# Performance work log

Hardware: AMD Instinct MI355X
Metric: run time of the kernel (lower is better)

Reference implementation:

```python
import jax, jax.numpy as jnp
import numpy as np

B, S, H, T = 32, 1024, 1024, 256
WINDOW = 2
ITERATIONS = 3


def setup_inputs() -> dict:
    key = jax.random.key(0)
    k1, k2, k3, k4, k5, k6 = jax.random.split(key, 6)
    token_feats = jax.random.normal(k1, (B, S, H), dtype=jnp.float32)
    unary_score = jax.random.normal(k2, (B, S, T), dtype=jnp.float32)
    lengths = jax.random.randint(k3, (B,), S // 2, S + 1)  # in [S/2, S]
    mask = (jnp.arange(S)[None, :] < lengths[:, None]).astype(jnp.float32)
    transitions = jax.random.normal(k4, (WINDOW, T, T), dtype=jnp.float32)
    start_transitions = jax.random.normal(k5, (WINDOW, T), dtype=jnp.float32)
    end_transitions = jax.random.normal(k6, (WINDOW, T), dtype=jnp.float32)
    return {
        "token_feats": token_feats,
        "unary_score": unary_score,
        "mask": mask,
        "transitions": transitions,
        "start_transitions": start_transitions,
        "end_transitions": end_transitions,
        "lengths": lengths,
    }


def reference(token_feats, unary_score, mask, transitions, start_transitions,
              end_transitions, lengths):
    # mask unary (and token_feats, as in original; token_feats is unused in
    # the plain-transitions second-order path)
    unary = unary_score * mask[..., None]        # [B,S,T]
    _ = token_feats * mask[..., None]
    q = unary
    batch_range = jnp.arange(q.shape[0])
    for _it in range(ITERATIONS):
        q = jax.nn.softmax(q, axis=-1)
        left_sum = jnp.zeros_like(q)
        right_sum = jnp.zeros_like(q)
        for j in range(1, WINDOW + 1):
            # message from left neighbor at distance j
            left_sum = left_sum.at[:, j:].add(
                jnp.einsum('nsa,ab->nsb', q[:, :-j], transitions[j - 1]))
            # message from right neighbor at distance j
            right_sum = right_sum.at[:, :-j].add(
                jnp.einsum('nsb,ab->nsa', q[:, j:], transitions[j - 1]))
            # end transitions scatter-add at position lengths - j
            right_sum = right_sum.at[batch_range, lengths - j].add(
                end_transitions[j - 1])
        msg = left_sum + right_sum
        # start transitions on first WINDOW positions (broadcast over batch)
        msg = msg.at[:, 0:WINDOW].add(start_transitions)
        q = unary + msg
        q = q * mask[..., None]
    return q
```

## Files before the change

kernel.cpp:

```cpp
#include <hip/hip_runtime.h>
#include <hip/hip_bf16.h>
#include <cstdint>


typedef __attribute__((ext_vector_type(4))) float f32x4;
typedef __attribute__((ext_vector_type(8))) short bf16x8;

__device__ __forceinline__ void load_lds16(const void* g, void* l) {
    __builtin_amdgcn_global_load_lds(
        (const __attribute__((address_space(1))) void*)g,
        (__attribute__((address_space(3))) void*)l, 16, 0, 0);
}

__global__ __launch_bounds__(256) void prep_wct(
    const float* __restrict__ trans,
    __hip_bfloat16* __restrict__ Pa, __hip_bfloat16* __restrict__ Pb,
    __hip_bfloat16* __restrict__ WcTt)
{
    int idx = blockIdx.x * 256 + threadIdx.x;
    if (idx < 32768) {
        int p = idx >> 10, sl = idx & 1023;
        int n = sl >> 2, cs = sl & 3;
        int gk = p * 4 + (cs ^ ((n >> 1) & 3));
        union { bf16x8 v; __hip_bfloat16 h[8]; } o;
        #pragma unroll
        for (int e = 0; e < 8; ++e) {
            int k = gk * 8 + e;
            int r = k >> 8, kk = k & 255;
            float v;
            if (r == 0)      v = trans[kk * 256 + n];
            else if (r == 1) v = trans[65536 + kk * 256 + n];
            else if (r == 2) v = trans[n * 256 + kk];
            else             v = trans[65536 + n * 256 + kk];
            o.h[e] = __float2bfloat16(v);
        }
        ((bf16x8*)WcTt)[idx] = o.v;
    } else if (idx < 40960) {
        int g = idx - 32768;
        __hip_bfloat16* P = (g & 4096) ? Pb : Pa;
        int rem = g & 4095;
        int b = rem >> 7, wr = (rem >> 5) & 3, ch = rem & 31;
        int row = b * 1028 + ((wr < 2) ? wr : 1024 + wr);
        bf16x8 z = {};
        *(bf16x8*)(P + row * 256 + ch * 8) = z;
    }
}

__global__ __launch_bounds__(512, 4) void mfvi_iter_k(
    const __hip_bfloat16* __restrict__ Pin,
    const __hip_bfloat16* __restrict__ WcTt,
    const float* __restrict__ unary, const int* __restrict__ lengths,
    const float* __restrict__ startT, const float* __restrict__ endT,
    __hip_bfloat16* __restrict__ Pout, float* __restrict__ out,
    int first_it, int final_it)
{
    __shared__ __hip_bfloat16 Ps[68 * 256];
    __shared__ __hip_bfloat16 Bs[2 * 256 * 32];
    __shared__ float redA[256];
    __shared__ float redB[256];

    int tid = threadIdx.x;
    int lane = tid & 63, w = tid >> 6;
    int cn = lane & 15, quad = lane >> 4;
    int wm = (w >> 2) * 32, wn = (w & 3) * 64;
    int nslice = w & 3;
    int tile = blockIdx.x;
    int b = tile >> 4, s0 = (tile & 15) << 6;
    int len = lengths[b];

    f32x4 acc[2][4] = {};

    if (first_it) {
        for (int q = 0; q < 9; ++q) {
            int r = w + q * 8;
            if (r >= 68) break;
            int s = s0 + r - 2;
            int ch = lane >> 1;
            int slot = (ch & ~7) | ((ch ^ r) & 7);
            char* dst = (char*)Ps + r * 512 + slot * 16 + (lane & 1) * 8;
            if (s >= 0 && s < 1024) {
                float mval = (s < len) ? 1.f : 0.f;
                float4 x = *((const float4*)(unary + ((size_t)((b << 10) + s)) * 256 + lane * 4));
                x.x *= mval; x.y *= mval; x.z *= mval; x.w *= mval;
                float mx = fmaxf(fmaxf(x.x, x.y), fmaxf(x.z, x.w));
                #pragma unroll
                for (int o = 32; o; o >>= 1) mx = fmaxf(mx, __shfl_xor(mx, o));
                float ea = __expf(x.x - mx), eb = __expf(x.y - mx);
                float ec = __expf(x.z - mx), ed = __expf(x.w - mx);
                float sum = ea + eb + ec + ed;
                #pragma unroll
                for (int o = 32; o; o >>= 1) sum += __shfl_xor(sum, o);
                float inv = 1.0f / sum;
                union { ushort4 u; __hip_bfloat16 h[4]; } o4;
                o4.h[0] = __float2bfloat16(ea * inv);
                o4.h[1] = __float2bfloat16(eb * inv);
                o4.h[2] = __float2bfloat16(ec * inv);
                o4.h[3] = __float2bfloat16(ed * inv);
                *((ushort4*)dst) = o4.u;
            } else {
                ushort4 z = {0, 0, 0, 0};
                *((ushort4*)dst) = z;
            }
        }
    } else {
        const char* Pbase = (const char*)(Pin + ((size_t)b * 1028 + s0) * 256);
        #pragma unroll
        for (int t = 0; t < 5; ++t) {
            int c = t * 512 + tid;
            if (t < 4 || tid < 128) {
                int row = c >> 5, ch = c & 31;
                int gch = (ch & ~7) | ((ch ^ row) & 7);
                load_lds16(Pbase + row * 512 + gch * 16, (char*)Ps + c * 16);
            }
        }
    }

    auto stageB = [&](int bb, int p) {
        #pragma unroll
        for (int c = 0; c < 2; ++c) {
            int sl = c * 512 + tid;
            load_lds16((const char*)WcTt + p * 16384 + sl * 16,
                       (char*)Bs + bb * 16384 + sl * 16);
        }
    };

    stageB(0, 0);
    __syncthreads();

    #pragma unroll 2
    for (int p = 0; p < 32; ++p) {
        if (p < 31) stageB((p + 1) & 1, p + 1);

        int region = p >> 3;
        int delta = (region == 0) ? -1 : (region == 1) ? -2
                  : (region == 2) ?  1 : 2;
        int gcb = (p & 7) * 4 + quad;

        bf16x8 af[2], bfv[4];
        #pragma unroll
        for (int i = 0; i < 2; ++i) {
            int r = wm + (i << 4) + cn + delta + 2;
            int slot = (gcb & ~7) | ((gcb ^ r) & 7);
            af[i] = *(const bf16x8*)((const char*)Ps + r * 512 + slot * 16);
        }
        #pragma unroll
        for (int j = 0; j < 4; ++j) {
            int n = wn + (j << 4) + cn;
            int cs = quad ^ ((n >> 1) & 3);
            bfv[j] = *(const bf16x8*)((const char*)Bs + (p & 1) * 16384 + n * 64 + cs * 16);
        }
        #pragma unroll
        for (int i = 0; i < 2; ++i)
            #pragma unroll
            for (int j = 0; j < 4; ++j)
                acc[i][j] = __builtin_amdgcn_mfma_f32_16x16x32_bf16(
                    af[i], bfv[j], acc[i][j], 0, 0, 0);

        __syncthreads();
    }

    #pragma unroll
    for (int i = 0; i < 2; ++i)
        #pragma unroll
        for (int j = 0; j < 4; ++j) {
            int n = wn + (j << 4) + cn;
            #pragma unroll
            for (int r = 0; r < 4; ++r) {
                int s = s0 + wm + (i << 4) + (quad << 2) + r;
                float x = acc[i][j][r];
                if (s == 0)       x += startT[n];
                if (s == 1)       x += startT[256 + n];
                if (s == len - 1) x += endT[n];
                if (s == len - 2) x += endT[256 + n];
                long idx = ((long)((b << 10) + s)) * 256 + n;
                x += unary[idx];
                acc[i][j][r] = (s < len) ? x : 0.f;
            }
        }

    if (final_it) {
        #pragma unroll
        for (int i = 0; i < 2; ++i)
            #pragma unroll
            for (int j = 0; j < 4; ++j) {
                int n = wn + (j << 4) + cn;
                #pragma unroll
                for (int r = 0; r < 4; ++r) {
                    int s = s0 + wm + (i << 4) + (quad << 2) + r;
                    out[((long)((b << 10) + s)) * 256 + n] = acc[i][j][r];
                }
            }
        return;
    }

    #pragma unroll
    for (int i = 0; i < 2; ++i)
        #pragma unroll
        for (int r = 0; r < 4; ++r) {
            float m4 = fmaxf(fmaxf(acc[i][0][r], acc[i][1][r]),
                             fmaxf(acc[i][2][r], acc[i][3][r]));
            m4 = fmaxf(m4, __shfl_xor(m4, 1));
            m4 = fmaxf(m4, __shfl_xor(m4, 2));
            m4 = fmaxf(m4, __shfl_xor(m4, 4));
            m4 = fmaxf(m4, __shfl_xor(m4, 8));
            if (cn == 0)
                redA[(nslice << 6) + wm + (i << 4) + (quad << 2) + r] = m4;
        }
    __syncthreads();
    float M[2][4];
    #pragma unroll
    for (int i = 0; i < 2; ++i)
        #pragma unroll
        for (int r = 0; r < 4; ++r) {
            int row = wm + (i << 4) + (quad << 2) + r;
            M[i][r] = fmaxf(fmaxf(redA[row], redA[64 + row]),
                            fmaxf(redA[128 + row], redA[192 + row]));
        }
    #pragma unroll
    for (int i = 0; i < 2; ++i)
        #pragma unroll
        for (int r = 0; r < 4; ++r) {
            float s4 = 0.f;
            #pragma unroll
            for (int j = 0; j < 4; ++j) {
                float e = __expf(acc[i][j][r] - M[i][r]);
                acc[i][j][r] = e;
                s4 += e;
            }
            s4 += __shfl_xor(s4, 1);
            s4 += __shfl_xor(s4, 2);
            s4 += __shfl_xor(s4, 4);
            s4 += __shfl_xor(s4, 8);
            if (cn == 0)
                redB[(nslice << 6) + wm + (i << 4) + (quad << 2) + r] = s4;
        }
    __syncthreads();
    #pragma unroll
    for (int i = 0; i < 2; ++i)
        #pragma unroll
        for (int r = 0; r < 4; ++r) {
            int row = wm + (i << 4) + (quad << 2) + r;
            float inv = 1.0f / (redB[row] + redB[64 + row] +
                                redB[128 + row] + redB[192 + row]);
            int s = s0 + row;
            #pragma unroll
            for (int j = 0; j < 4; ++j) {
                int n = wn + (j << 4) + cn;
                Pout[((size_t)b * 1028 + 2 + s) * 256 + n] =
                    __float2bfloat16(acc[i][j][r] * inv);
            }
        }
}

extern "C" void kernel_launch(void* const* d_in, const int* in_sizes, int n_in,
                              void* d_out, int out_size, void* d_ws, size_t ws_size,
                              hipStream_t stream) {
    const float* unary  = (const float*)d_in[1];
    const float* trans  = (const float*)d_in[3];
    const float* startT = (const float*)d_in[4];
    const float* endT   = (const float*)d_in[5];
    const int*   lens   = (const int*)d_in[6];

    char* ws = (char*)d_ws;
    __hip_bfloat16* Pa   = (__hip_bfloat16*)ws;
    __hip_bfloat16* Pb   = (__hip_bfloat16*)(ws + ((size_t)32 << 20));
    __hip_bfloat16* WcTt = (__hip_bfloat16*)(ws + ((size_t)64 << 20));
    float* out = (float*)d_out;

    prep_wct<<<dim3(160), dim3(256), 0, stream>>>(trans, Pa, Pb, WcTt);
    mfvi_iter_k<<<dim3(512), dim3(512), 0, stream>>>(Pa, WcTt, unary, lens, startT, endT, Pb, nullptr, 1, 0);
    mfvi_iter_k<<<dim3(512), dim3(512), 0, stream>>>(Pb, WcTt, unary, lens, startT, endT, Pa, nullptr, 0, 0);
    mfvi_iter_k<<<dim3(512), dim3(512), 0, stream>>>(Pa, WcTt, unary, lens, startT, endT, nullptr, out, 0, 1);
}
```

Measured before the change: 289.9 us.

## Fuse three MFVI iterations into one persistent kernel with neighbor halo flags

Replaces three per-iteration launches with a single kernel whose tiles keep their softmaxed q block in LDS across iterations. Tiles exchange only the two boundary rows with neighboring tiles through a small global halo buffer, synchronised by per-tile flags and spin-waits. This avoids writing and re-reading the full bf16 q tensor and the launch gaps between iterations. Tile indices are remapped so that neighboring tiles are spread across blocks. The scheme relies on all 512 blocks being co-resident, otherwise the spin-waits can deadlock, and each tile's halo reads wait on its neighbors finishing the previous iteration.

```diff
diff --git a/kernel.cpp b/kernel.cpp
--- a/kernel.cpp
+++ b/kernel.cpp
@@ -14,45 +14,38 @@
 
 __global__ __launch_bounds__(256) void prep_wct(
     const float* __restrict__ trans,
-    __hip_bfloat16* __restrict__ Pa, __hip_bfloat16* __restrict__ Pb,
-    __hip_bfloat16* __restrict__ WcTt)
+    __hip_bfloat16* __restrict__ WcTt, int* __restrict__ Flags)
 {
     int idx = blockIdx.x * 256 + threadIdx.x;
-    if (idx < 32768) {
-        int p = idx >> 10, sl = idx & 1023;
-        int n = sl >> 2, cs = sl & 3;
-        int gk = p * 4 + (cs ^ ((n >> 1) & 3));
-        union { bf16x8 v; __hip_bfloat16 h[8]; } o;
-        #pragma unroll
-        for (int e = 0; e < 8; ++e) {
-            int k = gk * 8 + e;
-            int r = k >> 8, kk = k & 255;
-            float v;
-            if (r == 0)      v = trans[kk * 256 + n];
-            else if (r == 1) v = trans[65536 + kk * 256 + n];
-            else if (r == 2) v = trans[n * 256 + kk];
-            else             v = trans[65536 + n * 256 + kk];
-            o.h[e] = __float2bfloat16(v);
-        }
-        ((bf16x8*)WcTt)[idx] = o.v;
-    } else if (idx < 40960) {
-        int g = idx - 32768;
-        __hip_bfloat16* P = (g & 4096) ? Pb : Pa;
-        int rem = g & 4095;
-        int b = rem >> 7, wr = (rem >> 5) & 3, ch = rem & 31;
-        int row = b * 1028 + ((wr < 2) ? wr : 1024 + wr);
-        bf16x8 z = {};
-        *(bf16x8*)(P + row * 256 + ch * 8) = z;
+    if (blockIdx.x == 0) {
+        Flags[threadIdx.x] = 0;
+        Flags[256 + threadIdx.x] = 0;
     }
+    int p = idx >> 10, sl = idx & 1023;
+    int n = sl >> 2, cs = sl & 3;
+    int gk = p * 4 + (cs ^ ((n >> 1) & 3));
+    union { bf16x8 v; __hip_bfloat16 h[8]; } o;
+    #pragma unroll
+    for (int e = 0; e < 8; ++e) {
+        int k = gk * 8 + e;
+        int r = k >> 8, kk = k & 255;
+        float v;
+        if (r == 0)      v = trans[kk * 256 + n];
+        else if (r == 1) v = trans[65536 + kk * 256 + n];
+        else if (r == 2) v = trans[n * 256 + kk];
+        else             v = trans[65536 + n * 256 + kk];
+        o.h[e] = __float2bfloat16(v);
+    }
+    ((bf16x8*)WcTt)[idx] = o.v;
 }
 
-__global__ __launch_bounds__(512, 4) void mfvi_iter_k(
-    const __hip_bfloat16* __restrict__ Pin,
+__global__ __launch_bounds__(512, 4) void mfvi_fused(
     const __hip_bfloat16* __restrict__ WcTt,
     const float* __restrict__ unary, const int* __restrict__ lengths,
     const float* __restrict__ startT, const float* __restrict__ endT,
-    __hip_bfloat16* __restrict__ Pout, float* __restrict__ out,
-    int first_it, int final_it)
+    __hip_bfloat16* Halo,
+    int* Flags,
+    float* __restrict__ out)
 {
     __shared__ __hip_bfloat16 Ps[68 * 256];
     __shared__ __hip_bfloat16 Bs[2 * 256 * 32];
@@ -64,56 +57,10 @@
     int cn = lane & 15, quad = lane >> 4;
     int wm = (w >> 2) * 32, wn = (w & 3) * 64;
     int nslice = w & 3;
-    int tile = blockIdx.x;
+    int tile = ((blockIdx.x & 7) << 6) | (blockIdx.x >> 3);
     int b = tile >> 4, s0 = (tile & 15) << 6;
     int len = lengths[b];
-
-    f32x4 acc[2][4] = {};
-
-    if (first_it) {
-        for (int q = 0; q < 9; ++q) {
-            int r = w + q * 8;
-            if (r >= 68) break;
-            int s = s0 + r - 2;
-            int ch = lane >> 1;
-            int slot = (ch & ~7) | ((ch ^ r) & 7);
-            char* dst = (char*)Ps + r * 512 + slot * 16 + (lane & 1) * 8;
-            if (s >= 0 && s < 1024) {
-                float mval = (s < len) ? 1.f : 0.f;
-                float4 x = *((const float4*)(unary + ((size_t)((b << 10) + s)) * 256 + lane * 4));
-                x.x *= mval; x.y *= mval; x.z *= mval; x.w *= mval;
-                float mx = fmaxf(fmaxf(x.x, x.y), fmaxf(x.z, x.w));
-                #pragma unroll
-                for (int o = 32; o; o >>= 1) mx = fmaxf(mx, __shfl_xor(mx, o));
-                float ea = __expf(x.x - mx), eb = __expf(x.y - mx);
-                float ec = __expf(x.z - mx), ed = __expf(x.w - mx);
-                float sum = ea + eb + ec + ed;
-                #pragma unroll
-                for (int o = 32; o; o >>= 1) sum += __shfl_xor(sum, o);
-                float inv = 1.0f / sum;
-                union { ushort4 u; __hip_bfloat16 h[4]; } o4;
-                o4.h[0] = __float2bfloat16(ea * inv);
-                o4.h[1] = __float2bfloat16(eb * inv);
-                o4.h[2] = __float2bfloat16(ec * inv);
-                o4.h[3] = __float2bfloat16(ed * inv);
-                *((ushort4*)dst) = o4.u;
-            } else {
-                ushort4 z = {0, 0, 0, 0};
-                *((ushort4*)dst) = z;
-            }
-        }
-    } else {
-        const char* Pbase = (const char*)(Pin + ((size_t)b * 1028 + s0) * 256);
-        #pragma unroll
-        for (int t = 0; t < 5; ++t) {
-            int c = t * 512 + tid;
-            if (t < 4 || tid < 128) {
-                int row = c >> 5, ch = c & 31;
-                int gch = (ch & ~7) | ((ch ^ row) & 7);
-                load_lds16(Pbase + row * 512 + gch * 16, (char*)Ps + c * 16);
-            }
-        }
-    }
+    int tpos = tile & 15;
 
     auto stageB = [&](int bb, int p) {
         #pragma unroll
@@ -124,132 +71,213 @@
         }
     };
 
-    stageB(0, 0);
-    __syncthreads();
-
-    #pragma unroll 2
-    for (int p = 0; p < 32; ++p) {
-        if (p < 31) stageB((p + 1) & 1, p + 1);
-
-        int region = p >> 3;
-        int delta = (region == 0) ? -1 : (region == 1) ? -2
-                  : (region == 2) ?  1 : 2;
-        int gcb = (p & 7) * 4 + quad;
-
-        bf16x8 af[2], bfv[4];
-        #pragma unroll
-        for (int i = 0; i < 2; ++i) {
-            int r = wm + (i << 4) + cn + delta + 2;
-            int slot = (gcb & ~7) | ((gcb ^ r) & 7);
-            af[i] = *(const bf16x8*)((const char*)Ps + r * 512 + slot * 16);
-        }
-        #pragma unroll
-        for (int j = 0; j < 4; ++j) {
-            int n = wn + (j << 4) + cn;
-            int cs = quad ^ ((n >> 1) & 3);
-            bfv[j] = *(const bf16x8*)((const char*)Bs + (p & 1) * 16384 + n * 64 + cs * 16);
-        }
-        #pragma unroll
-        for (int i = 0; i < 2; ++i)
-            #pragma unroll
-            for (int j = 0; j < 4; ++j)
-                acc[i][j] = __builtin_amdgcn_mfma_f32_16x16x32_bf16(
-                    af[i], bfv[j], acc[i][j], 0, 0, 0);
-
-        __syncthreads();
-    }
-
-    #pragma unroll
-    for (int i = 0; i < 2; ++i)
-        #pragma unroll
-        for (int j = 0; j < 4; ++j) {
-            int n = wn + (j << 4) + cn;
-            #pragma unroll
-            for (int r = 0; r < 4; ++r) {
-                int s = s0 + wm + (i << 4) + (quad << 2) + r;
-                float x = acc[i][j][r];
-                if (s == 0)       x += startT[n];
-                if (s == 1)       x += startT[256 + n];
-                if (s == len - 1) x += endT[n];
-                if (s == len - 2) x += endT[256 + n];
-                long idx = ((long)((b << 10) + s)) * 256 + n;
-                x += unary[idx];
-                acc[i][j][r] = (s < len) ? x : 0.f;
-            }
-        }
-
-    if (final_it) {
-        #pragma unroll
-        for (int i = 0; i < 2; ++i)
+    #pragma unroll 1
+    for (int it = 1; it <= 3; ++it) {
+        if (it == 1) {
+            for (int q = 0; q < 9; ++q) {
+                int r = w + q * 8;
+                if (r >= 68) break;
+                int s = s0 + r - 2;
+                int ch = lane >> 1;
+                int slot = (ch & ~7) | ((ch ^ r) & 7);
+                char* dst = (char*)Ps + r * 512 + slot * 16 + (lane & 1) * 8;
+                if (s >= 0 && s < 1024) {
+                    float mval = (s < len) ? 1.f : 0.f;
+                    float4 x = *((const float4*)(unary + ((size_t)((b << 10) + s)) * 256 + lane * 4));
+                    x.x *= mval; x.y *= mval; x.z *= mval; x.w *= mval;
+                    float mx = fmaxf(fmaxf(x.x, x.y), fmaxf(x.z, x.w));
+                    #pragma unroll
+                    for (int o = 32; o; o >>= 1) mx = fmaxf(mx, __shfl_xor(mx, o));
+                    float ea = __expf(x.x - mx), eb = __expf(x.y - mx);
+                    float ec = __expf(x.z - mx), ed = __expf(x.w - mx);
+                    float sum = ea + eb + ec + ed;
+                    #pragma unroll
+                    for (int o = 32; o; o >>= 1) sum += __shfl_xor(sum, o);
+                    float inv = 1.0f / sum;
+                    union { ushort4 u; __hip_bfloat16 h[4]; } o4;
+                    o4.h[0] = __float2bfloat16(ea * inv);
+                    o4.h[1] = __float2bfloat16(eb * inv);
+                    o4.h[2] = __float2bfloat16(ec * inv);
+                    o4.h[3] = __float2bfloat16(ed * inv);
+                    *((ushort4*)dst) = o4.u;
+                } else {
+                    ushort4 z = {0, 0, 0, 0};
+                    *((ushort4*)dst) = z;
+                }
+            }
+        } else {
+            if (tid == 0) {
+                if (tpos != 0)
+                    while (atomicAdd(Flags + tile - 1, 0) < it - 1)
+                        __builtin_amdgcn_s_sleep(1);
+                if (tpos != 15)
+                    while (atomicAdd(Flags + tile + 1, 0) < it - 1)
+                        __builtin_amdgcn_s_sleep(1);
+            }
+            __syncthreads();
+            __threadfence();
+            if (tid < 128) {
+                int r_idx = tid >> 5, ch = tid & 31;
+                int pr = (r_idx < 2) ? r_idx : 64 + r_idx;
+                bool left = (r_idx < 2);
+                bool valid = left ? (tpos != 0) : (tpos != 15);
+                int nbr = left ? tile - 1 : tile + 1;
+                int src_row = left ? 2 + r_idx : r_idx - 2;
+                int gch = (ch & ~7) | ((ch ^ pr) & 7);
+                bf16x8 v = {};
+                if (valid)
+                    v = *(const bf16x8*)(Halo +
+                        ((((size_t)(it - 2) * 512 + nbr) * 4 + src_row) * 256) + gch * 8);
+                *(bf16x8*)((char*)Ps + (pr * 32 + ch) * 16) = v;
+            }
+        }
+
+        stageB(0, 0);
+        __syncthreads();
+
+        f32x4 acc[2][4] = {};
+
+        #pragma unroll 2
+        for (int p = 0; p < 32; ++p) {
+            if (p < 31) stageB((p + 1) & 1, p + 1);
+
+            int region = p >> 3;
+            int delta = (region == 0) ? -1 : (region == 1) ? -2
+                      : (region == 2) ?  1 : 2;
+            int gcb = (p & 7) * 4 + quad;
+
+            bf16x8 af[2], bfv[4];
+            #pragma unroll
+            for (int i = 0; i < 2; ++i) {
+                int r = wm + (i << 4) + cn + delta + 2;
+                int slot = (gcb & ~7) | ((gcb ^ r) & 7);
+                af[i] = *(const bf16x8*)((const char*)Ps + r * 512 + slot * 16);
+            }
             #pragma unroll
             for (int j = 0; j < 4; ++j) {
                 int n = wn + (j << 4) + cn;
+                int cs = quad ^ ((n >> 1) & 3);
+                bfv[j] = *(const bf16x8*)((const char*)Bs + (p & 1) * 16384 + n * 64 + cs * 16);
+            }
+            #pragma unroll
+            for (int i = 0; i < 2; ++i)
+                #pragma unroll
+                for (int j = 0; j < 4; ++j)
+                    acc[i][j] = __builtin_amdgcn_mfma_f32_16x16x32_bf16(
+                        af[i], bfv[j], acc[i][j], 0, 0, 0);
+
+            __syncthreads();
+        }
+
+        #pragma unroll
+        for (int i = 0; i < 2; ++i)
+            #pragma unroll
+            for (int j = 0; j < 4; ++j) {
+                int n = wn + (j << 4) + cn;
                 #pragma unroll
                 for (int r = 0; r < 4; ++r) {
                     int s = s0 + wm + (i << 4) + (quad << 2) + r;
-                    out[((long)((b << 10) + s)) * 256 + n] = acc[i][j][r];
-                }
-            }
-        return;
+                    float x = acc[i][j][r];
+                    if (s == 0)       x += startT[n];
+                    if (s == 1)       x += startT[256 + n];
+                    if (s == len - 1) x += endT[n];
+                    if (s == len - 2) x += endT[256 + n];
+                    long idx = ((long)((b << 10) + s)) * 256 + n;
+                    x += unary[idx];
+                    acc[i][j][r] = (s < len) ? x : 0.f;
+                }
+            }
+
+        if (it == 3) {
+            #pragma unroll
+            for (int i = 0; i < 2; ++i)
+                #pragma unroll
+                for (int j = 0; j < 4; ++j) {
+                    int n = wn + (j << 4) + cn;
+                    #pragma unroll
+                    for (int r = 0; r < 4; ++r) {
+                        int s = s0 + wm + (i << 4) + (quad << 2) + r;
+                        out[((long)((b << 10) + s)) * 256 + n] = acc[i][j][r];
+                    }
+                }
+            return;
+        }
+
+        #pragma unroll
+        for (int i = 0; i < 2; ++i)
+            #pragma unroll
+            for (int r = 0; r < 4; ++r) {
+                float m4 = fmaxf(fmaxf(acc[i][0][r], acc[i][1][r]),
+                                 fmaxf(acc[i][2][r], acc[i][3][r]));
+                m4 = fmaxf(m4, __shfl_xor(m4, 1));
+                m4 = fmaxf(m4, __shfl_xor(m4, 2));
+                m4 = fmaxf(m4, __shfl_xor(m4, 4));
+                m4 = fmaxf(m4, __shfl_xor(m4, 8));
+                if (cn == 0)
+                    redA[(nslice << 6) + wm + (i << 4) + (quad << 2) + r] = m4;
+            }
+        __syncthreads();
+        float M[2][4];
+        #pragma unroll
+        for (int i = 0; i < 2; ++i)
+            #pragma unroll
+            for (int r = 0; r < 4; ++r) {
+                int row = wm + (i << 4) + (quad << 2) + r;
+                M[i][r] = fmaxf(fmaxf(redA[row], redA[64 + row]),
+                                fmaxf(redA[128 + row], redA[192 + row]));
+            }
+        #pragma unroll
+        for (int i = 0; i < 2; ++i)
+            #pragma unroll
+            for (int r = 0; r < 4; ++r) {
+                float s4 = 0.f;
+                #pragma unroll
+                for (int j = 0; j < 4; ++j) {
+                    float e = __expf(acc[i][j][r] - M[i][r]);
+                    acc[i][j][r] = e;
+                    s4 += e;
+                }
+                s4 += __shfl_xor(s4, 1);
+                s4 += __shfl_xor(s4, 2);
+                s4 += __shfl_xor(s4, 4);
+                s4 += __shfl_xor(s4, 8);
+                if (cn == 0)
+                    redB[(nslice << 6) + wm + (i << 4) + (quad << 2) + r] = s4;
+            }
+        __syncthreads();
+
+        #pragma unroll
+        for (int i = 0; i < 2; ++i)
+            #pragma unroll
+            for (int r = 0; r < 4; ++r) {
+                int row = wm + (i << 4) + (quad << 2) + r;
+                float inv = 1.0f / (redB[row] + redB[64 + row] +
+                                    redB[128 + row] + redB[192 + row]);
+                int pr = row + 2;
+                #pragma unroll
+                for (int j = 0; j < 4; ++j) {
+                    int n = wn + (j << 4) + cn;
+                    int ch = n >> 3;
+                    int slot = (ch & ~7) | ((ch ^ pr) & 7);
+                    *((__hip_bfloat16*)((char*)Ps + pr * 512 + slot * 16 + (n & 7) * 2)) =
+                        __float2bfloat16(acc[i][j][r] * inv);
+                }
+            }
+        __syncthreads();
+
+        if (tid < 128) {
+            int r_idx = tid >> 5, ch = tid & 31;
+            int pr = (r_idx < 2) ? 2 + r_idx : 62 + r_idx;
+            int slot = (ch & ~7) | ((ch ^ pr) & 7);
+            bf16x8 v = *(const bf16x8*)((const char*)Ps + (pr * 32 + slot) * 16);
+            *(bf16x8*)(Halo + (((size_t)(it - 1) * 512 + tile) * 4 + r_idx) * 256 + ch * 8) = v;
+        }
+        __syncthreads();
+        if (tid == 0) {
+            __threadfence();
+            atomicExch(Flags + tile, it);
+        }
     }
-
-    #pragma unroll
-    for (int i = 0; i < 2; ++i)
-        #pragma unroll
-        for (int r = 0; r < 4; ++r) {
-            float m4 = fmaxf(fmaxf(acc[i][0][r], acc[i][1][r]),
-                             fmaxf(acc[i][2][r], acc[i][3][r]));
-            m4 = fmaxf(m4, __shfl_xor(m4, 1));
-            m4 = fmaxf(m4, __shfl_xor(m4, 2));
-            m4 = fmaxf(m4, __shfl_xor(m4, 4));
-            m4 = fmaxf(m4, __shfl_xor(m4, 8));
-            if (cn == 0)
-                redA[(nslice << 6) + wm + (i << 4) + (quad << 2) + r] = m4;
-        }
-    __syncthreads();
-    float M[2][4];
-    #pragma unroll
-    for (int i = 0; i < 2; ++i)
-        #pragma unroll
-        for (int r = 0; r < 4; ++r) {
-            int row = wm + (i << 4) + (quad << 2) + r;
-            M[i][r] = fmaxf(fmaxf(redA[row], redA[64 + row]),
-                            fmaxf(redA[128 + row], redA[192 + row]));
-        }
-    #pragma unroll
-    for (int i = 0; i < 2; ++i)
-        #pragma unroll
-        for (int r = 0; r < 4; ++r) {
-            float s4 = 0.f;
-            #pragma unroll
-            for (int j = 0; j < 4; ++j) {
-                float e = __expf(acc[i][j][r] - M[i][r]);
-                acc[i][j][r] = e;
-                s4 += e;
-            }
-            s4 += __shfl_xor(s4, 1);
-            s4 += __shfl_xor(s4, 2);
-            s4 += __shfl_xor(s4, 4);
-            s4 += __shfl_xor(s4, 8);
-            if (cn == 0)
-                redB[(nslice << 6) + wm + (i << 4) + (quad << 2) + r] = s4;
-        }
-    __syncthreads();
-    #pragma unroll
-    for (int i = 0; i < 2; ++i)
-        #pragma unroll
-        for (int r = 0; r < 4; ++r) {
-            int row = wm + (i << 4) + (quad << 2) + r;
-            float inv = 1.0f / (redB[row] + redB[64 + row] +
-                                redB[128 + row] + redB[192 + row]);
-            int s = s0 + row;
-            #pragma unroll
-            for (int j = 0; j < 4; ++j) {
-                int n = wn + (j << 4) + cn;
-                Pout[((size_t)b * 1028 + 2 + s) * 256 + n] =
-                    __float2bfloat16(acc[i][j][r] * inv);
-            }
-        }
 }
 
 extern "C" void kernel_launch(void* const* d_in, const int* in_sizes, int n_in,
@@ -262,13 +290,11 @@
     const int*   lens   = (const int*)d_in[6];
 
     char* ws = (char*)d_ws;
-    __hip_bfloat16* Pa   = (__hip_bfloat16*)ws;
-    __hip_bfloat16* Pb   = (__hip_bfloat16*)(ws + ((size_t)32 << 20));
-    __hip_bfloat16* WcTt = (__hip_bfloat16*)(ws + ((size_t)64 << 20));
+    __hip_bfloat16* WcTt  = (__hip_bfloat16*)ws;
+    __hip_bfloat16* Halo  = (__hip_bfloat16*)(ws + ((size_t)1 << 20));
+    int*            Flags = (int*)(ws + ((size_t)4 << 20));
     float* out = (float*)d_out;
 
-    prep_wct<<<dim3(160), dim3(256), 0, stream>>>(trans, Pa, Pb, WcTt);
-    mfvi_iter_k<<<dim3(512), dim3(512), 0, stream>>>(Pa, WcTt, unary, lens, startT, endT, Pb, nullptr, 1, 0);
-    mfvi_iter_k<<<dim3(512), dim3(512), 0, stream>>>(Pb, WcTt, unary, lens, startT, endT, Pa, nullptr, 0, 0);
-    mfvi_iter_k<<<dim3(512), dim3(512), 0, stream>>>(Pa, WcTt, unary, lens, startT, endT, nullptr, out, 0, 1);
+    prep_wct<<<dim3(128), dim3(256), 0, stream>>>(trans, WcTt, Flags);
+    mfvi_fused<<<dim3(512), dim3(512), 0, stream>>>(WcTt, unary, lens, startT, endT, Halo, Flags, out);
 }
```

After: 502.4 us. 1.73x slower.

## Load transition B-fragments directly from global memory instead of LDS staging

Applied to the files above, without the earlier changes.

The transposed transition matrix is now stored in plain row-major [n][k] layout, and each lane reads its B fragments straight from global/L2 memory. This replaces the double-buffered LDS staging, which needed a __syncthreads every k-step. The k-loop is fully unrolled over regions and chunks with no barriers, and launch bounds drop to 2 blocks per SM to allow more registers. The trade-off is heavier global/L2 traffic, since each wave re-reads the 256 KB weight matrix, and lower occupancy.

```diff
diff --git a/kernel.cpp b/kernel.cpp
--- a/kernel.cpp
+++ b/kernel.cpp
@@ -15,17 +15,15 @@
 __global__ __launch_bounds__(256) void prep_wct(
     const float* __restrict__ trans,
     __hip_bfloat16* __restrict__ Pa, __hip_bfloat16* __restrict__ Pb,
-    __hip_bfloat16* __restrict__ WcTt)
+    __hip_bfloat16* __restrict__ WcT)
 {
     int idx = blockIdx.x * 256 + threadIdx.x;
     if (idx < 32768) {
-        int p = idx >> 10, sl = idx & 1023;
-        int n = sl >> 2, cs = sl & 3;
-        int gk = p * 4 + (cs ^ ((n >> 1) & 3));
+        int n = idx >> 7, c = idx & 127;
         union { bf16x8 v; __hip_bfloat16 h[8]; } o;
         #pragma unroll
         for (int e = 0; e < 8; ++e) {
-            int k = gk * 8 + e;
+            int k = c * 8 + e;
             int r = k >> 8, kk = k & 255;
             float v;
             if (r == 0)      v = trans[kk * 256 + n];
@@ -34,7 +32,7 @@
             else             v = trans[65536 + n * 256 + kk];
             o.h[e] = __float2bfloat16(v);
         }
-        ((bf16x8*)WcTt)[idx] = o.v;
+        ((bf16x8*)WcT)[idx] = o.v;
     } else if (idx < 40960) {
         int g = idx - 32768;
         __hip_bfloat16* P = (g & 4096) ? Pb : Pa;
@@ -46,16 +44,15 @@
     }
 }
 
-__global__ __launch_bounds__(512, 4) void mfvi_iter_k(
+__global__ __launch_bounds__(512, 2) void mfvi_iter_k(
     const __hip_bfloat16* __restrict__ Pin,
-    const __hip_bfloat16* __restrict__ WcTt,
+    const __hip_bfloat16* __restrict__ WcT,
     const float* __restrict__ unary, const int* __restrict__ lengths,
     const float* __restrict__ startT, const float* __restrict__ endT,
     __hip_bfloat16* __restrict__ Pout, float* __restrict__ out,
     int first_it, int final_it)
 {
     __shared__ __hip_bfloat16 Ps[68 * 256];
-    __shared__ __hip_bfloat16 Bs[2 * 256 * 32];
     __shared__ float redA[256];
     __shared__ float redB[256];
 
@@ -67,8 +64,6 @@
     int tile = blockIdx.x;
     int b = tile >> 4, s0 = (tile & 15) << 6;
     int len = lengths[b];
-
-    f32x4 acc[2][4] = {};
 
     if (first_it) {
         for (int q = 0; q < 9; ++q) {
@@ -114,49 +109,40 @@
             }
         }
     }
-
-    auto stageB = [&](int bb, int p) {
-        #pragma unroll
-        for (int c = 0; c < 2; ++c) {
-            int sl = c * 512 + tid;
-            load_lds16((const char*)WcTt + p * 16384 + sl * 16,
-                       (char*)Bs + bb * 16384 + sl * 16);
-        }
-    };
-
-    stageB(0, 0);
     __syncthreads();
 
-    #pragma unroll 2
-    for (int p = 0; p < 32; ++p) {
-        if (p < 31) stageB((p + 1) & 1, p + 1);
-
-        int region = p >> 3;
+    const char* Bb[4];
+    #pragma unroll
+    for (int j = 0; j < 4; ++j)
+        Bb[j] = (const char*)WcT + (wn + (j << 4) + cn) * 2048 + quad * 16;
+
+    f32x4 acc[2][4] = {};
+
+    #pragma unroll
+    for (int region = 0; region < 4; ++region) {
         int delta = (region == 0) ? -1 : (region == 1) ? -2
                   : (region == 2) ?  1 : 2;
-        int gcb = (p & 7) * 4 + quad;
-
-        bf16x8 af[2], bfv[4];
-        #pragma unroll
-        for (int i = 0; i < 2; ++i) {
-            int r = wm + (i << 4) + cn + delta + 2;
-            int slot = (gcb & ~7) | ((gcb ^ r) & 7);
-            af[i] = *(const bf16x8*)((const char*)Ps + r * 512 + slot * 16);
-        }
-        #pragma unroll
-        for (int j = 0; j < 4; ++j) {
-            int n = wn + (j << 4) + cn;
-            int cs = quad ^ ((n >> 1) & 3);
-            bfv[j] = *(const bf16x8*)((const char*)Bs + (p & 1) * 16384 + n * 64 + cs * 16);
-        }
-        #pragma unroll
-        for (int i = 0; i < 2; ++i)
+        int r0 = wm + cn + delta + 2;
+        #pragma unroll
+        for (int q = 0; q < 8; ++q) {
+            int gcb = q * 4 + quad;
+            bf16x8 af[2], bfv[4];
+            #pragma unroll
+            for (int i = 0; i < 2; ++i) {
+                int r = r0 + (i << 4);
+                int slot = (gcb & ~7) | ((gcb ^ r) & 7);
+                af[i] = *(const bf16x8*)((const char*)Ps + r * 512 + slot * 16);
+            }
             #pragma unroll
             for (int j = 0; j < 4; ++j)
-                acc[i][j] = __builtin_amdgcn_mfma_f32_16x16x32_bf16(
-                    af[i], bfv[j], acc[i][j], 0, 0, 0);
-
-        __syncthreads();
+                bfv[j] = *(const bf16x8*)(Bb[j] + region * 512 + q * 64);
+            #pragma unroll
+            for (int i = 0; i < 2; ++i)
+                #pragma unroll
+                for (int j = 0; j < 4; ++j)
+                    acc[i][j] = __builtin_amdgcn_mfma_f32_16x16x32_bf16(
+                        af[i], bfv[j], acc[i][j], 0, 0, 0);
+        }
     }
 
     #pragma unroll
@@ -262,13 +248,13 @@
     const int*   lens   = (const int*)d_in[6];
 
     char* ws = (char*)d_ws;
-    __hip_bfloat16* Pa   = (__hip_bfloat16*)ws;
-    __hip_bfloat16* Pb   = (__hip_bfloat16*)(ws + ((size_t)32 << 20));
-    __hip_bfloat16* WcTt = (__hip_bfloat16*)(ws + ((size_t)64 << 20));
+    __hip_bfloat16* Pa  = (__hip_bfloat16*)ws;
+    __hip_bfloat16* Pb  = (__hip_bfloat16*)(ws + ((size_t)32 << 20));
+    __hip_bfloat16* WcT = (__hip_bfloat16*)(ws + ((size_t)64 << 20));
     float* out = (float*)d_out;
 
-    prep_wct<<<dim3(160), dim3(256), 0, stream>>>(trans, Pa, Pb, WcTt);
-    mfvi_iter_k<<<dim3(512), dim3(512), 0, stream>>>(Pa, WcTt, unary, lens, startT, endT, Pb, nullptr, 1, 0);
-    mfvi_iter_k<<<dim3(512), dim3(512), 0, stream>>>(Pb, WcTt, unary, lens, startT, endT, Pa, nullptr, 0, 0);
-    mfvi_iter_k<<<dim3(512), dim3(512), 0, stream>>>(Pa, WcTt, unary, lens, startT, endT, nullptr, out, 0, 1);
-}
+    prep_wct<<<dim3(160), dim3(256), 0, stream>>>(trans, Pa, Pb, WcT);
+    mfvi_iter_k<<<dim3(512), dim3(512), 0, stream>>>(Pa, WcT, unary, lens, startT, endT, Pb, nullptr, 1, 0);
+    mfvi_iter_k<<<dim3(512), dim3(512), 0, stream>>>(Pb, WcT, unary, lens, startT, endT, Pa, nullptr, 0, 0);
+    mfvi_iter_k<<<dim3(512), dim3(512), 0, stream>>>(Pa, WcT, unary, lens, startT, endT, nullptr, out, 0, 1);
+}
```

Result: slower. 400.6 us (+38.2%).

## Deepen B-tile prefetch pipeline with explicit vmcnt waits and split barriers

Applied to the files above, without the earlier changes.

Restructures the K loop so two B stages are in flight. Each step waits with an explicit vmcnt count before a barrier, reads its fragments from LDS, then issues the next global-to-LDS stage into the buffer it just drained before running the MFMAs. Wave priority is raised around the MFMA block, and the loop is fully unrolled. The goal is to hide global load latency behind compute. In exchange it uses two barriers per step, and correctness depends on hand-counted vmcnt values.

```diff
diff --git a/kernel.cpp b/kernel.cpp
--- a/kernel.cpp
+++ b/kernel.cpp
@@ -67,8 +67,6 @@
     int tile = blockIdx.x;
     int b = tile >> 4, s0 = (tile & 15) << 6;
     int len = lengths[b];
-
-    f32x4 acc[2][4] = {};
 
     if (first_it) {
         for (int q = 0; q < 9; ++q) {
@@ -114,6 +112,7 @@
             }
         }
     }
+    __syncthreads();
 
     auto stageB = [&](int bb, int p) {
         #pragma unroll
@@ -125,39 +124,49 @@
     };
 
     stageB(0, 0);
-    __syncthreads();
-
-    #pragma unroll 2
-    for (int p = 0; p < 32; ++p) {
-        if (p < 31) stageB((p + 1) & 1, p + 1);
-
-        int region = p >> 3;
-        int delta = (region == 0) ? -1 : (region == 1) ? -2
-                  : (region == 2) ?  1 : 2;
-        int gcb = (p & 7) * 4 + quad;
-
-        bf16x8 af[2], bfv[4];
-        #pragma unroll
-        for (int i = 0; i < 2; ++i) {
-            int r = wm + (i << 4) + cn + delta + 2;
-            int slot = (gcb & ~7) | ((gcb ^ r) & 7);
-            af[i] = *(const bf16x8*)((const char*)Ps + r * 512 + slot * 16);
-        }
-        #pragma unroll
-        for (int j = 0; j < 4; ++j) {
-            int n = wn + (j << 4) + cn;
-            int cs = quad ^ ((n >> 1) & 3);
-            bfv[j] = *(const bf16x8*)((const char*)Bs + (p & 1) * 16384 + n * 64 + cs * 16);
-        }
-        #pragma unroll
-        for (int i = 0; i < 2; ++i)
-            #pragma unroll
-            for (int j = 0; j < 4; ++j)
-                acc[i][j] = __builtin_amdgcn_mfma_f32_16x16x32_bf16(
-                    af[i], bfv[j], acc[i][j], 0, 0, 0);
-
-        __syncthreads();
-    }
+    stageB(1, 1);
+
+    f32x4 acc[2][4] = {};
+
+#define K_STEP(P, VMC, DOSTAGE) do {                                         \
+    asm volatile("s_waitcnt vmcnt(" #VMC ")" ::: "memory");                  \
+    __builtin_amdgcn_s_barrier();                                            \
+    int region = (P) >> 3;                                                   \
+    int delta = (region == 0) ? -1 : (region == 1) ? -2                      \
+              : (region == 2) ?  1 : 2;                                      \
+    int gcb = ((P) & 7) * 4 + quad;                                          \
+    bf16x8 af[2], bfv[4];                                                    \
+    _Pragma("unroll")                                                        \
+    for (int i = 0; i < 2; ++i) {                                            \
+        int r = wm + (i << 4) + cn + delta + 2;                              \
+        int slot = (gcb & ~7) | ((gcb ^ r) & 7);                             \
+        af[i] = *(const bf16x8*)((const char*)Ps + r * 512 + slot * 16);     \
+    }                                                                        \
+    _Pragma("unroll")                                                        \
+    for (int j = 0; j < 4; ++j) {                                            \
+        int n = wn + (j << 4) + cn;                                          \
+        int cs = quad ^ ((n >> 1) & 3);                                      \
+        bfv[j] = *(const bf16x8*)((const char*)Bs + ((P) & 1) * 16384        \
+                                  + n * 64 + cs * 16);                       \
+    }                                                                        \
+    asm volatile("s_waitcnt lgkmcnt(0)" ::: "memory");                       \
+    __builtin_amdgcn_s_barrier();                                            \
+    if (DOSTAGE) stageB(((P) & 1), (P) + 2);                                 \
+    __builtin_amdgcn_s_setprio(1);                                           \
+    _Pragma("unroll")                                                        \
+    for (int i = 0; i < 2; ++i)                                              \
+        _Pragma("unroll")                                                    \
+        for (int j = 0; j < 4; ++j)                                          \
+            acc[i][j] = __builtin_amdgcn_mfma_f32_16x16x32_bf16(             \
+                af[i], bfv[j], acc[i][j], 0, 0, 0);                          \
+    __builtin_amdgcn_s_setprio(0);                                           \
+} while (0)
+
+    #pragma unroll
+    for (int p = 0; p < 30; ++p) K_STEP(p, 2, true);
+    K_STEP(30, 2, false);
+    K_STEP(31, 0, false);
+#undef K_STEP
 
     #pragma unroll
     for (int i = 0; i < 2; ++i)
```

New measurement: 278.7 us. 3.9% less time.
